# Kernel tuning notes

Measured on AMD Instinct MI355X. Metric: run time of the kernel, lower is better.

The kernel has to match this reference:

```python
import jax, jax.numpy as jnp
import numpy as np

NBITS = 4
GROUP = 128
K = 4096   # in_features
N = 4096   # out_features
M = 4096   # flattened batch*seq tokens
EPS = 32 // NBITS  # elements per packed int32 = 8
MASK = (1 << NBITS) - 1  # unpack_mask = 15


def setup_inputs() -> dict:
    key = jax.random.key(0)
    k1, k2, k3, k4, k5 = jax.random.split(key, 5)
    x = jax.random.normal(k1, (M, K), dtype=jnp.float32)
    # raw 4-bit quantized weights, layout [K, N] (i.e. W_q.t() from the torch module)
    nib = jax.random.randint(k2, (K, N), 0, 1 << NBITS, dtype=jnp.int32)
    # pack EPS nibbles per int32 along K, matching pack(): element j gets shift j*NBITS
    nib = nib.reshape(K // EPS, EPS, N)
    shifts = (jnp.arange(EPS, dtype=jnp.int32) * NBITS)[None, :, None]
    parts = nib << shifts  # disjoint bit ranges
    W_q_packed = parts[:, 0]
    for j in range(1, EPS):
        W_q_packed = W_q_packed | parts[:, j]
    W_q_packed = W_q_packed.astype(jnp.int32)  # [K//EPS, N]
    # group-wise scales/zeros: [K//GROUP, N] (scales.view(N,-1).t() layout)
    scales = (jax.random.uniform(k3, (K // GROUP, N), dtype=jnp.float32) + 0.5) * 0.01
    zeros = jax.random.uniform(k4, (K // GROUP, N), dtype=jnp.float32) * MASK
    bias = jax.random.normal(k5, (N,), dtype=jnp.float32) * 0.1
    return {"x": x, "W_q_packed": W_q_packed, "scales": scales, "zeros": zeros, "bias": bias}


def reference(x, W_q_packed, scales, zeros, bias):
    # unpack: w[k, n] = (packed[k//EPS, n] >> ((k % EPS) * NBITS)) & MASK
    shifts = (jnp.arange(EPS, dtype=jnp.int32) * NBITS)[None, :, None]
    w = (W_q_packed[:, None, :] >> shifts) & MASK  # [K//EPS, EPS, N]
    w = w.reshape(K, N).astype(jnp.float32)
    # group-wise asymmetric dequant (W_group_mode == 3): W = (w - z) * s
    s = jnp.repeat(scales, GROUP, axis=0)  # [K, N]
    z = jnp.repeat(zeros, GROUP, axis=0)   # [K, N]
    W = (w - z) * s
    out = x @ W + bias  # [M, N]
    return out
```

## Files before the change

kernel.cpp:

```cpp
#include <hip/hip_runtime.h>
#include <stdint.h>


#define M_DIM 4096
#define N_DIM 4096
#define K_DIM 4096

typedef __attribute__((ext_vector_type(8))) short short8;
typedef __attribute__((ext_vector_type(4))) float f32x4;

__device__ __forceinline__ unsigned short f2bf(float f) {
  uint32_t u = __builtin_bit_cast(uint32_t, f);
  u += 0x7fffu + ((u >> 16) & 1u);
  return (unsigned short)(u >> 16);
}

__global__ __launch_bounds__(256) void prep_kernel(const float* __restrict__ x,
                                                   unsigned short* __restrict__ xb,
                                                   const int* __restrict__ Wq,
                                                   const float* __restrict__ scales,
                                                   const float* __restrict__ zeros,
                                                   unsigned short* __restrict__ wt) {
  __shared__ uint4 Ts[32 * 64];
  const int tid = threadIdx.x;
  if (blockIdx.x < 2048) {
    const int total = (M_DIM * K_DIM) / 8;
    const float4* x4 = (const float4*)x;
    uint4* o8 = (uint4*)xb;
#pragma unroll
    for (int p = 0; p < 4; ++p) {
      int i = (p * 2048 + blockIdx.x) * 256 + tid;
      if (i < total) {
        float4 a = x4[2 * i], b = x4[2 * i + 1];
        uint4 o;
        o.x = (uint32_t)f2bf(a.x) | ((uint32_t)f2bf(a.y) << 16);
        o.y = (uint32_t)f2bf(a.z) | ((uint32_t)f2bf(a.w) << 16);
        o.z = (uint32_t)f2bf(b.x) | ((uint32_t)f2bf(b.y) << 16);
        o.w = (uint32_t)f2bf(b.z) | ((uint32_t)f2bf(b.w) << 16);
        o8[i] = o;
      }
    }
    return;
  }
  const int blk = blockIdx.x - 2048;
  const int n0 = (blk & 127) * 32;
  const int gk0 = (blk >> 7) * 64;

#pragma unroll
  for (int p = 0; p < 8; ++p) {
    int e = p * 256 + tid;
    int n_l = e & 31;
    int gk_l = e >> 5;
    int gk = gk0 + gk_l;
    int n = n0 + n_l;
    int g = gk >> 4;
    uint32_t q = (uint32_t)Wq[gk * N_DIM + n];
    float s = scales[g * N_DIM + n];
    float z = zeros[g * N_DIM + n];
    unsigned short b[8];
#pragma unroll
    for (int j = 0; j < 8; ++j) {
      float f = ((float)((q >> (4 * j)) & 15u) - z) * s;
      b[j] = f2bf(f);
    }
    uint4 cell;
    cell.x = (uint32_t)b[0] | ((uint32_t)b[1] << 16);
    cell.y = (uint32_t)b[2] | ((uint32_t)b[3] << 16);
    cell.z = (uint32_t)b[4] | ((uint32_t)b[5] << 16);
    cell.w = (uint32_t)b[6] | ((uint32_t)b[7] << 16);
    Ts[n_l * 64 + (gk_l ^ (n_l & 7))] = cell;
  }
  __syncthreads();
  uint4* dst = (uint4*)wt;
#pragma unroll
  for (int p = 0; p < 8; ++p) {
    int n_l = p * 4 + (tid >> 6);
    int gk_l = tid & 63;
    uint4 cell = Ts[n_l * 64 + (gk_l ^ (n_l & 7))];
    dst[(size_t)(n0 + n_l) * (K_DIM / 8) + (gk0 + gk_l)] = cell;
  }
}


#define STAGE4(DST, SRC)                                                         \
  {                                                                              \
    _Pragma("unroll") for (int j = 0; j < 4; ++j)                                \
        __builtin_amdgcn_global_load_lds(                                        \
            (const __attribute__((address_space(1))) void*)((SRC) +              \
                                                            (size_t)j * 64 * K_DIM), \
            (__attribute__((address_space(3))) void*)((DST) + tid + j * 512),    \
            16, 0, 0);                                                           \
  }

#define LOADA(QM)                                                                \
  {                                                                              \
    _Pragma("unroll") for (int mi = 0; mi < 4; ++mi) {                           \
      af[mi][0] = ASb[a_base + ((QM) * 4 + mi) * 128 + kx0];                     \
      af[mi][1] = ASb[a_base + ((QM) * 4 + mi) * 128 + kx1];                     \
    }                                                                            \
  }

#define LOADB(QN)                                                                \
  {                                                                              \
    _Pragma("unroll") for (int ni = 0; ni < 2; ++ni) {                           \
      bv[ni][0] = BSb[b_base + ((QN) * 2 + ni) * 128 + kx0];                     \
      bv[ni][1] = BSb[b_base + ((QN) * 2 + ni) * 128 + kx1];                     \
    }                                                                            \
  }

#define MFMA16(QM, QN)                                                           \
  {                                                                              \
    _Pragma("unroll") for (int mi = 0; mi < 4; ++mi)                             \
        _Pragma("unroll") for (int ni = 0; ni < 2; ++ni) {                       \
      acc[(QM) * 4 + mi][(QN) * 2 + ni] = __builtin_amdgcn_mfma_f32_16x16x32_bf16( \
          af[mi][0], bv[ni][0], acc[(QM) * 4 + mi][(QN) * 2 + ni], 0, 0, 0);     \
      acc[(QM) * 4 + mi][(QN) * 2 + ni] = __builtin_amdgcn_mfma_f32_16x16x32_bf16( \
          af[mi][1], bv[ni][1], acc[(QM) * 4 + mi][(QN) * 2 + ni], 0, 0, 0);     \
    }                                                                            \
  }

#define PHASE_MFMA(QM, QN)                                                       \
  {                                                                              \
    __builtin_amdgcn_s_barrier();                                                \
    __builtin_amdgcn_s_setprio(1);                                               \
    MFMA16(QM, QN);                                                              \
    __builtin_amdgcn_s_setprio(0);                                               \
    __builtin_amdgcn_s_barrier();                                                \
  }

__global__ __launch_bounds__(512, 2) void gemm_bt_kernel(
    const unsigned short* __restrict__ A, const unsigned short* __restrict__ Bt,
    const float* __restrict__ bias, float* __restrict__ C) {
  __shared__ short8 As[2 * 2048];
  __shared__ short8 Bs[2 * 2048];

  const int tid = threadIdx.x;
  const int lane = tid & 63;
  const int w = tid >> 6;
  const int wm = w >> 2;
  const int wn = w & 3;

  const int b = blockIdx.x;
  const int xcd = b & 7;
  const int loc = b >> 3;
  const int nt = xcd * 2 + (loc & 1);
  const int mt = loc >> 1;
  const int m0 = mt * 256;
  const int n0 = nt * 256;

  const int srow = tid >> 3;
  const int skc = (tid & 7) ^ (srow & 7);
  const unsigned short* Ablk = A + (size_t)m0 * K_DIM + (size_t)srow * K_DIM + skc * 8;
  const unsigned short* Bblk = Bt + (size_t)n0 * K_DIM + (size_t)srow * K_DIM + skc * 8;

  const int fr = lane & 15;
  const int fc = lane >> 4;
  const int frx = fr & 7;
  const int a_base = (wm * 128 + fr) * 8;
  const int b_base = (wn * 64 + fr) * 8;
  const int kx0 = fc ^ frx;
  const int kx1 = (4 + fc) ^ frx;

  f32x4 acc[8][4] = {};
  short8 af[4][2];
  short8 bv[2][2];

  STAGE4(As, Ablk);
  STAGE4(Bs, Bblk);
  asm volatile("s_waitcnt vmcnt(0)" ::: "memory");
  __builtin_amdgcn_s_barrier();

  for (int kt = 0; kt < K_DIM / 64; ++kt) {
    const int cur = kt & 1;
    const short8* ASb = As + cur * 2048;
    const short8* BSb = Bs + cur * 2048;
    short8* Anx = As + (cur ^ 1) * 2048;
    short8* Bnx = Bs + (cur ^ 1) * 2048;
    const bool pf = (kt + 1 < K_DIM / 64);
    const size_t knext = (size_t)(kt + 1) * 64;

    LOADA(0);
    LOADB(0);
    if (pf) STAGE4(Anx, Ablk + knext);
    PHASE_MFMA(0, 0);

    LOADB(1);
    if (pf) STAGE4(Bnx, Bblk + knext);
    PHASE_MFMA(0, 1);

    LOADA(1);
    PHASE_MFMA(1, 1);

    LOADB(0);
    __builtin_amdgcn_s_barrier();
    __builtin_amdgcn_s_setprio(1);
    MFMA16(1, 0);
    __builtin_amdgcn_s_setprio(0);
    asm volatile("s_waitcnt vmcnt(0)" ::: "memory");
    __builtin_amdgcn_s_barrier();
  }

  const int rr = (lane >> 4) * 4;
#pragma unroll
  for (int ni = 0; ni < 4; ++ni) {
    const int gn = n0 + wn * 64 + ni * 16 + fr;
    const float bvv = bias[gn];
#pragma unroll
    for (int mi = 0; mi < 8; ++mi) {
      const int gm = m0 + wm * 128 + mi * 16 + rr;
#pragma unroll
      for (int r = 0; r < 4; ++r)
        C[(size_t)(gm + r) * N_DIM + gn] = acc[mi][ni][r] + bvv;
    }
  }
}

extern "C" void kernel_launch(void* const* d_in, const int* in_sizes, int n_in,
                              void* d_out, int out_size, void* d_ws, size_t ws_size,
                              hipStream_t stream) {
  const float* x = (const float*)d_in[0];
  const int* wq = (const int*)d_in[1];
  const float* sc = (const float*)d_in[2];
  const float* zr = (const float*)d_in[3];
  const float* bias = (const float*)d_in[4];
  float* out = (float*)d_out;

  unsigned short* xb = (unsigned short*)d_ws;
  unsigned short* wt = (unsigned short*)((char*)d_ws + (size_t)M_DIM * K_DIM * 2);

  prep_kernel<<<dim3(3072), dim3(256), 0, stream>>>(x, xb, wq, sc, zr, wt);
  gemm_bt_kernel<<<dim3(256), dim3(512), 0, stream>>>(xb, wt, bias, out);
}
```

Measured before the change: 266.8 us.

## Prefetch two K-tiles ahead and drop per-phase barriers in GEMM loop

The GEMM main loop now issues global-to-LDS loads two iterations ahead into the buffer just consumed, waiting only on the older batch with vmcnt(8). The per-phase double barriers around each MFMA group are gone, and all B fragments are loaded once per iteration. This leaves one barrier pair per K-tile instead of eight, so more memory latency is hidden and there are fewer sync stalls. In exchange it holds more B registers, which can raise register pressure at two blocks per CU, and the ordering of waits and barriers becomes more delicate.

Result: no change. 269.6 us (+1.0%).

```diff
diff --git a/kernel.cpp b/kernel.cpp
--- a/kernel.cpp
+++ b/kernel.cpp
@@ -5,6 +5,7 @@
 #define M_DIM 4096
 #define N_DIM 4096
 #define K_DIM 4096
+#define NT (K_DIM / 64)
 
 typedef __attribute__((ext_vector_type(8))) short short8;
 typedef __attribute__((ext_vector_type(4))) float f32x4;
@@ -100,32 +101,25 @@
     }                                                                            \
   }
 
-#define LOADB(QN)                                                                \
-  {                                                                              \
-    _Pragma("unroll") for (int ni = 0; ni < 2; ++ni) {                           \
-      bv[ni][0] = BSb[b_base + ((QN) * 2 + ni) * 128 + kx0];                     \
-      bv[ni][1] = BSb[b_base + ((QN) * 2 + ni) * 128 + kx1];                     \
+#define LOADBALL                                                                 \
+  {                                                                              \
+    _Pragma("unroll") for (int nn = 0; nn < 4; ++nn) {                           \
+      bv[nn][0] = BSb[b_base + nn * 128 + kx0];                                  \
+      bv[nn][1] = BSb[b_base + nn * 128 + kx1];                                  \
     }                                                                            \
   }
 
 #define MFMA16(QM, QN)                                                           \
   {                                                                              \
+    __builtin_amdgcn_s_setprio(1);                                               \
     _Pragma("unroll") for (int mi = 0; mi < 4; ++mi)                             \
         _Pragma("unroll") for (int ni = 0; ni < 2; ++ni) {                       \
       acc[(QM) * 4 + mi][(QN) * 2 + ni] = __builtin_amdgcn_mfma_f32_16x16x32_bf16( \
-          af[mi][0], bv[ni][0], acc[(QM) * 4 + mi][(QN) * 2 + ni], 0, 0, 0);     \
+          af[mi][0], bv[(QN) * 2 + ni][0], acc[(QM) * 4 + mi][(QN) * 2 + ni], 0, 0, 0); \
       acc[(QM) * 4 + mi][(QN) * 2 + ni] = __builtin_amdgcn_mfma_f32_16x16x32_bf16( \
-          af[mi][1], bv[ni][1], acc[(QM) * 4 + mi][(QN) * 2 + ni], 0, 0, 0);     \
+          af[mi][1], bv[(QN) * 2 + ni][1], acc[(QM) * 4 + mi][(QN) * 2 + ni], 0, 0, 0); \
     }                                                                            \
-  }
-
-#define PHASE_MFMA(QM, QN)                                                       \
-  {                                                                              \
-    __builtin_amdgcn_s_barrier();                                                \
-    __builtin_amdgcn_s_setprio(1);                                               \
-    MFMA16(QM, QN);                                                              \
     __builtin_amdgcn_s_setprio(0);                                               \
-    __builtin_amdgcn_s_barrier();                                                \
   }
 
 __global__ __launch_bounds__(512, 2) void gemm_bt_kernel(
@@ -163,40 +157,40 @@
 
   f32x4 acc[8][4] = {};
   short8 af[4][2];
-  short8 bv[2][2];
+  short8 bv[4][2];
 
   STAGE4(As, Ablk);
   STAGE4(Bs, Bblk);
-  asm volatile("s_waitcnt vmcnt(0)" ::: "memory");
+  STAGE4(As + 2048, Ablk + 64);
+  STAGE4(Bs + 2048, Bblk + 64);
+  asm volatile("s_waitcnt vmcnt(8)" ::: "memory");
+  __builtin_amdgcn_sched_barrier(0);
   __builtin_amdgcn_s_barrier();
 
-  for (int kt = 0; kt < K_DIM / 64; ++kt) {
+  for (int kt = 0; kt < NT; ++kt) {
     const int cur = kt & 1;
     const short8* ASb = As + cur * 2048;
     const short8* BSb = Bs + cur * 2048;
-    short8* Anx = As + (cur ^ 1) * 2048;
-    short8* Bnx = Bs + (cur ^ 1) * 2048;
-    const bool pf = (kt + 1 < K_DIM / 64);
-    const size_t knext = (size_t)(kt + 1) * 64;
 
     LOADA(0);
-    LOADB(0);
-    if (pf) STAGE4(Anx, Ablk + knext);
-    PHASE_MFMA(0, 0);
-
-    LOADB(1);
-    if (pf) STAGE4(Bnx, Bblk + knext);
-    PHASE_MFMA(0, 1);
-
+    LOADBALL;
+    MFMA16(0, 0);
+    MFMA16(0, 1);
     LOADA(1);
-    PHASE_MFMA(1, 1);
-
-    LOADB(0);
+    MFMA16(1, 1);
+    MFMA16(1, 0);
+
+    asm volatile("s_waitcnt lgkmcnt(0)" ::: "memory");
+    __builtin_amdgcn_sched_barrier(0);
     __builtin_amdgcn_s_barrier();
-    __builtin_amdgcn_s_setprio(1);
-    MFMA16(1, 0);
-    __builtin_amdgcn_s_setprio(0);
-    asm volatile("s_waitcnt vmcnt(0)" ::: "memory");
+    if (kt + 2 < NT) {
+      STAGE4(As + cur * 2048, Ablk + (size_t)(kt + 2) * 64);
+      STAGE4(Bs + cur * 2048, Bblk + (size_t)(kt + 2) * 64);
+      asm volatile("s_waitcnt vmcnt(8)" ::: "memory");
+    } else {
+      asm volatile("s_waitcnt vmcnt(0)" ::: "memory");
+    }
+    __builtin_amdgcn_sched_barrier(0);
     __builtin_amdgcn_s_barrier();
   }
 
```
